# Kernel optimization log

Hardware: AMD Instinct MI355X
Metric: run time of the kernel (lower is better)

## Reference

```python
import jax, jax.numpy as jnp
import numpy as np

BS = 2
EMBED = 256
NH = 8
NL = 4
NP = 4
HD = EMBED // NH
SHAPES = [(128, 128), (64, 64), (32, 32), (16, 16)]
NQ = sum(h * w for h, w in SHAPES)  # 21760


def setup_inputs() -> dict:
    key = jax.random.key(0)
    ks = jax.random.split(key, 12)
    s = 1.0 / np.sqrt(EMBED)
    return {
        "query": jax.random.normal(ks[0], (BS, NQ, EMBED), jnp.float32),
        "reference_points": jax.random.uniform(ks[1], (BS, NQ, NL, 2), jnp.float32),
        "value": jax.random.normal(ks[2], (BS, NQ, EMBED), jnp.float32),
        "W_off": jax.random.normal(ks[3], (EMBED, NH * NL * NP * 2), jnp.float32) * 0.01,
        "b_off": jax.random.normal(ks[4], (NH * NL * NP * 2,), jnp.float32) * 0.5,
        "W_attn": jax.random.normal(ks[5], (EMBED, NH * NL * NP), jnp.float32) * 0.02,
        "b_attn": jnp.zeros((NH * NL * NP,), jnp.float32),
        "W_v": jax.random.normal(ks[6], (EMBED, EMBED), jnp.float32) * s,
        "b_v": jnp.zeros((EMBED,), jnp.float32),
        "W_out": jax.random.normal(ks[7], (EMBED, EMBED), jnp.float32) * s,
        "b_out": jnp.zeros((EMBED,), jnp.float32),
        "value_spatial_shapes": np.asarray(SHAPES, dtype=np.int64),
    }


def _ms_deform_attn(value, shapes, loc, aw):
    # value: [bs,V,nh,d]; loc: [bs,nq,nh,L,P,2] in [0,1]; aw: [bs,nq,nh,L,P]
    bs, V, nh, d = value.shape
    nq = loc.shape[1]
    out = jnp.zeros((bs, nq, nh, d), value.dtype)
    start = 0
    b_idx = jnp.arange(bs)[:, None, None, None]
    h_idx = jnp.arange(nh)[None, None, :, None]
    for l, (H, W) in enumerate(shapes):
        H, W = int(H), int(W)
        v = value[:, start:start + H * W].reshape(bs, H, W, nh, d)
        start += H * W
        g = 2.0 * loc[:, :, :, l] - 1.0  # [bs,nq,nh,P,2], grid_sample convention
        # align_corners=False pixel coordinates
        x = ((g[..., 0] + 1.0) * W - 1.0) * 0.5
        y = ((g[..., 1] + 1.0) * H - 1.0) * 0.5
        x0 = jnp.floor(x); y0 = jnp.floor(y)
        wx1 = x - x0; wx0 = 1.0 - wx1
        wy1 = y - y0; wy0 = 1.0 - wy1

        def gather(yi, xi):
            inb = (yi >= 0) & (yi < H) & (xi >= 0) & (xi < W)
            yc = jnp.clip(yi, 0, H - 1).astype(jnp.int32)
            xc = jnp.clip(xi, 0, W - 1).astype(jnp.int32)
            vals = v[b_idx, yc, xc, h_idx]  # [bs,nq,nh,P,d]
            return vals * inb[..., None].astype(v.dtype)

        samp = (gather(y0, x0) * (wy0 * wx0)[..., None]
                + gather(y0, x0 + 1) * (wy0 * wx1)[..., None]
                + gather(y0 + 1, x0) * (wy1 * wx0)[..., None]
                + gather(y0 + 1, x0 + 1) * (wy1 * wx1)[..., None])
        out = out + jnp.einsum('bqhpd,bqhp->bqhd', samp, aw[:, :, :, l])
    return out.reshape(bs, nq, nh * d)


def reference(query, reference_points, value, W_off, b_off, W_attn, b_attn,
              W_v, b_v, W_out, b_out, value_spatial_shapes):
    shapes = np.asarray(value_spatial_shapes)  # static [L,2]
    bs, nq, _ = query.shape
    v = (value @ W_v + b_v).reshape(bs, -1, NH, HD)
    off = (query @ W_off + b_off).reshape(bs, nq, NH, NL, NP, 2)
    aw = (query @ W_attn + b_attn).reshape(bs, nq, NH, NL * NP)
    aw = jax.nn.softmax(aw, axis=-1).reshape(bs, nq, NH, NL, NP)
    # offset normalizer: (W,H) per level
    norm = jnp.asarray(shapes[:, ::-1].astype(np.float32))  # [L,2]
    loc = reference_points[:, :, None, :, None, :] + off / norm[None, None, None, :, None, :]
    out = _ms_deform_attn(v, shapes, loc, aw)
    return out @ W_out + b_out
```

## Files before the change

### kernel.cpp

```cpp
#include <hip/hip_runtime.h>
#include <math.h>

#define BS 2
#define NQ 21760
#define V_LEN 21760
#define EMBED 256
#define NH 8
#define NL 4
#define NP 4
#define HD 32

typedef __bf16 bf16;
typedef __bf16 bf16x8 __attribute__((ext_vector_type(8)));
typedef __bf16 bf16x4 __attribute__((ext_vector_type(4)));
typedef float f32x4 __attribute__((ext_vector_type(4)));
typedef float f32x2 __attribute__((ext_vector_type(2)));
typedef unsigned int u32;

#define GLOAD_LDS16(gp, lp_) \
    __builtin_amdgcn_global_load_lds( \
        (const __attribute__((address_space(1))) unsigned int*)(gp), \
        (__attribute__((address_space(3))) unsigned int*)(lp_), 16, 0, 0)

__global__ __launch_bounds__(256) void cast_all(
    const float* __restrict__ W_v, const float* __restrict__ W_off,
    const float* __restrict__ W_attn, const float* __restrict__ W_out,
    const float* __restrict__ b_off, const float* __restrict__ b_attn,
    bf16* __restrict__ WTv, bf16* __restrict__ WToa, bf16* __restrict__ WTu,
    float* __restrict__ bcat)
{
    const int bid = blockIdx.x;
    const int tid = threadIdx.x;
    if (bid == 56) {
        if (tid < 384) bcat[tid] = (tid < 256) ? b_off[tid] : b_attn[tid - 256];
        return;
    }
    const float* W; bf16* WT; int N, tile;
    if (bid < 16)      { W = W_v;    WT = WTv;           N = 256; tile = bid; }
    else if (bid < 32) { W = W_off;  WT = WToa;          N = 256; tile = bid - 16; }
    else if (bid < 40) { W = W_attn; WT = WToa + 65536;  N = 128; tile = bid - 32; }
    else               { W = W_out;  WT = WTu;           N = 256; tile = bid - 40; }
    const int ntn = N >> 6;
    const int k0 = (tile / ntn) * 64, n0 = (tile % ntn) * 64;

    __shared__ float lds[64][65];
    const int c = tid & 63, r4 = tid >> 6;
    #pragma unroll
    for (int p = 0; p < 16; p++) {
        int rr = r4 + p * 4;
        lds[rr][c] = W[(size_t)(k0 + rr) * N + n0 + c];
    }
    __syncthreads();
    #pragma unroll
    for (int p = 0; p < 16; p++) {
        int i = r4 + p * 4;
        WT[(size_t)(n0 + i) * 256 + k0 + c] = (bf16)lds[c][i];
    }
}

template<bool A_F32, int OUT_MODE>
__global__ __launch_bounds__(256) void gemm_mfma(
    const void* __restrict__ Av, const bf16* __restrict__ WT,
    const float* __restrict__ bias, void* __restrict__ Cv,
    int N, int K, int ntn)
{
    const int nmt = gridDim.x / ntn;
    const int bmt = blockIdx.x % nmt;
    const int bnt = blockIdx.x / nmt;
    const int bm = bmt * 128, bn = bnt * 128;

    __shared__ __align__(16) bf16 Bs[2][128 * 32];
    __shared__ __align__(16) unsigned char AsRaw[2][A_F32 ? 128 * 32 * 4
                                                         : 128 * 32 * 2];

    const int tid = threadIdx.x;
    const int lane = tid & 63, wv = tid >> 6;
    const int wr = wv >> 1, wc = wv & 1;
    const int quad = lane >> 4, l16 = lane & 15;

    f32x4 acc[4][4];
    #pragma unroll
    for (int i = 0; i < 4; i++)
        #pragma unroll
        for (int j = 0; j < 4; j++)
            acc[i][j] = (f32x4){0.f, 0.f, 0.f, 0.f};

    const int b_row = tid >> 2, b_chunk = tid & 3;
    const int a_row8 = tid >> 3, a_phys = tid & 7;
    constexpr int NB = A_F32 ? 6 : 4;

    auto stage = [&](int buf, int k0) {
        if constexpr (A_F32) {
            const float* A = (const float*)Av;
            #pragma unroll
            for (int p = 0; p < 4; p++) {
                int row = a_row8 + p * 32;
                int csrc = a_phys ^ (row & 7);
                GLOAD_LDS16(&A[(size_t)(bm + row) * K + k0 + csrc * 4],
                            &AsRaw[buf][p * 4096 + tid * 16]);
            }
        } else {
            const bf16* A = (const bf16*)Av;
            #pragma unroll
            for (int p = 0; p < 2; p++) {
                int row = b_row + p * 64;
                GLOAD_LDS16(&A[(size_t)(bm + row) * K + k0 + b_chunk * 8],
                            &AsRaw[buf][p * 4096 + tid * 16]);
            }
        }
        #pragma unroll
        for (int p = 0; p < 2; p++) {
            int row = b_row + p * 64;
            GLOAD_LDS16(&WT[(size_t)(bn + row) * K + k0 + b_chunk * 8],
                        (unsigned char*)&Bs[buf][0] + p * 4096 + tid * 16);
        }
    };

    const int nt = K >> 5;
    stage(0, 0);
    int cur = 0;
    for (int t = 0; t < nt; t++) {
        __builtin_amdgcn_s_barrier();
        if (t + 1 < nt) {
            stage(cur ^ 1, (t + 1) << 5);
            asm volatile("s_waitcnt vmcnt(%0)" :: "n"(NB) : "memory");
        } else {
            asm volatile("s_waitcnt vmcnt(0)" ::: "memory");
        }
        __builtin_amdgcn_s_barrier();

        bf16x8 af[4], bfr[4];
        if constexpr (A_F32) {
            const float* Asf = (const float*)&AsRaw[cur][0];
            #pragma unroll
            for (int mi = 0; mi < 4; mi++) {
                int r = wr * 64 + mi * 16 + l16;
                int g = r & 7;
                f32x4 u0 = *(const f32x4*)&Asf[r * 32 + ((2 * quad) ^ g) * 4];
                f32x4 u1 = *(const f32x4*)&Asf[r * 32 + ((2 * quad + 1) ^ g) * 4];
                bf16x8 hh;
                hh[0] = (bf16)u0[0]; hh[1] = (bf16)u0[1]; hh[2] = (bf16)u0[2]; hh[3] = (bf16)u0[3];
                hh[4] = (bf16)u1[0]; hh[5] = (bf16)u1[1]; hh[6] = (bf16)u1[2]; hh[7] = (bf16)u1[3];
                af[mi] = hh;
            }
        } else {
            const bf16* Asb = (const bf16*)&AsRaw[cur][0];
            #pragma unroll
            for (int mi = 0; mi < 4; mi++) {
                int r = wr * 64 + mi * 16 + l16;
                af[mi] = *(const bf16x8*)&Asb[r * 32 + quad * 8];
            }
        }
        #pragma unroll
        for (int ni = 0; ni < 4; ni++) {
            int r = wc * 64 + ni * 16 + l16;
            bfr[ni] = *(const bf16x8*)&Bs[cur][r * 32 + quad * 8];
        }
        #pragma unroll
        for (int mi = 0; mi < 4; mi++)
            #pragma unroll
            for (int ni = 0; ni < 4; ni++)
                acc[mi][ni] = __builtin_amdgcn_mfma_f32_16x16x32_bf16(
                    af[mi], bfr[ni], acc[mi][ni], 0, 0, 0);
        cur ^= 1;
    }

    #pragma unroll
    for (int mi = 0; mi < 4; mi++) {
        #pragma unroll
        for (int ni = 0; ni < 4; ni++) {
            const int col = bn + wc * 64 + ni * 16 + l16;
            const int row0 = bm + wr * 64 + mi * 16 + quad * 4;
            const float bc = bias[col];
            #pragma unroll
            for (int r = 0; r < 4; r++) {
                float v = acc[mi][ni][r] + bc;
                if constexpr (OUT_MODE == 0) {
                    ((float*)Cv)[(size_t)(row0 + r) * N + col] = v;
                } else if constexpr (OUT_MODE == 1) {
                    ((bf16*)Cv)[(size_t)(row0 + r) * N + col] = (bf16)v;
                } else {
                    int rv = row0 + r;
                    int bb = (rv >= V_LEN) ? 1 : 0;
                    int vv = rv - bb * V_LEN;
                    ((bf16*)Cv)[((size_t)(bb * NH + (col >> 5)) * V_LEN + vv) * 32
                                + (col & 31)] = (bf16)v;
                }
            }
        }
    }
}

__device__ inline void acc8(const uint4& rr, float ww,
                            f32x2& a01, f32x2& a23, f32x2& a45, f32x2& a67)
{
    f32x2 v;
    v[0] = __uint_as_float(rr.x << 16); v[1] = __uint_as_float(rr.x & 0xFFFF0000u); a01 += v * ww;
    v[0] = __uint_as_float(rr.y << 16); v[1] = __uint_as_float(rr.y & 0xFFFF0000u); a23 += v * ww;
    v[0] = __uint_as_float(rr.z << 16); v[1] = __uint_as_float(rr.z & 0xFFFF0000u); a45 += v * ww;
    v[0] = __uint_as_float(rr.w << 16); v[1] = __uint_as_float(rr.w & 0xFFFF0000u); a67 += v * ww;
}

__global__ __launch_bounds__(256) void deform_head(
    const bf16* __restrict__ vproj, const float* __restrict__ offaw,
    const float* __restrict__ refp, bf16* __restrict__ sampled)
{
    const int gid = blockIdx.x;
    const int idx8 = gid & 7;
    const int mid = gid >> 3;
    const int qg = mid % (NQ / 16);
    const int hsel = mid / (NQ / 16);
    const int h = (idx8 >> 1) + (hsel << 2);
    const int b = idx8 & 1;

    const int wv = threadIdx.x >> 6;
    const int t = threadIdx.x & 63;
    const int qq = t >> 4, s = t & 15;
    const int q = qg * 16 + wv * 4 + qq;
    const int bq = b * NQ + q;
    const int wq = wv * 4 + qq;

    __shared__ __align__(16) float s_w[16][16][4];
    __shared__ int s_idx[16][16];

    const float* row = offaw + (size_t)bq * 384;

    float lg = row[256 + h * 16 + s];
    float m = lg;
    m = fmaxf(m, __shfl_xor(m, 1));
    m = fmaxf(m, __shfl_xor(m, 2));
    m = fmaxf(m, __shfl_xor(m, 4));
    m = fmaxf(m, __shfl_xor(m, 8));
    float ev = __expf(lg - m);
    float ssum = ev;
    ssum += __shfl_xor(ssum, 1);
    ssum += __shfl_xor(ssum, 2);
    ssum += __shfl_xor(ssum, 4);
    ssum += __shfl_xor(ssum, 8);
    float aw = ev * (1.0f / ssum);

    {
        int l = s >> 2;
        int Wl = 128 >> l, Hl = Wl;
        int st = (l == 0) ? 0 : (l == 1) ? 16384 : (l == 2) ? 20480 : 21504;
        float2 rp = *(const float2*)&refp[((size_t)bq * 4 + l) * 2];
        float2 oxy = *(const float2*)&row[h * 32 + s * 2];
        float fW = (float)Wl, fH = (float)Hl;
        float x = (rp.x + oxy.x / fW) * fW - 0.5f;
        float y = (rp.y + oxy.y / fH) * fH - 0.5f;
        float xf = floorf(x), yf = floorf(y);
        int x0 = (int)xf, y0 = (int)yf;
        float wx1 = x - xf, wx0 = 1.f - wx1;
        float wy1 = y - yf, wy0 = 1.f - wy1;
        float wx0p = ((x0 >= 0) && (x0 < Wl)) ? wx0 : 0.f;
        float wx1p = ((x0 + 1 >= 0) && (x0 + 1 < Wl)) ? wx1 : 0.f;
        float wy0p = ((y0 >= 0) && (y0 < Hl)) ? wy0 : 0.f;
        float wy1p = ((y0 + 1 >= 0) && (y0 + 1 < Hl)) ? wy1 : 0.f;
        int px = min(max(x0, 0), Wl - 2), py = min(max(y0, 0), Hl - 2);
        int cx0 = min(max(x0, 0), Wl - 1), cx1 = min(max(x0 + 1, 0), Wl - 1);
        int cy0 = min(max(y0, 0), Hl - 1), cy1 = min(max(y0 + 1, 0), Hl - 1);
        float sx0 = ((cx0 == px) ? wx0p : 0.f) + ((cx1 == px) ? wx1p : 0.f);
        float sx1 = ((cx0 == px + 1) ? wx0p : 0.f) + ((cx1 == px + 1) ? wx1p : 0.f);
        float sy0 = ((cy0 == py) ? wy0p : 0.f) + ((cy1 == py) ? wy1p : 0.f);
        float sy1 = ((cy0 == py + 1) ? wy0p : 0.f) + ((cy1 == py + 1) ? wy1p : 0.f);
        s_idx[wq][s] = st + py * Wl + px;
        s_w[wq][s][0] = sy0 * sx0 * aw;
        s_w[wq][s][1] = sy0 * sx1 * aw;
        s_w[wq][s][2] = sy1 * sx0 * aw;
        s_w[wq][s][3] = sy1 * sx1 * aw;
    }

    const int chgrp = t & 3;
    const int xslot = (t >> 2) & 1;
    const int rowsel = (t >> 3) & 1;
    const int widx = rowsel * 2 + xslot;
    const bf16* vb = vproj + (size_t)(b * NH + h) * V_LEN * 32;

    f32x2 a01 = {0.f, 0.f}, a23 = {0.f, 0.f}, a45 = {0.f, 0.f}, a67 = {0.f, 0.f};
    #pragma unroll
    for (int i = 0; i < 16; i++) {
        const int Wl = 128 >> (i >> 2);
        int base = s_idx[wq][i];
        float w = s_w[wq][i][widx];
        const bf16* p = vb + (size_t)(base + rowsel * Wl + xslot) * 32 + chgrp * 8;
        uint4 r = *(const uint4*)p;
        acc8(r, w, a01, a23, a45, a67);
    }

    float sarr[8] = {a01[0], a01[1], a23[0], a23[1], a45[0], a45[1], a67[0], a67[1]};
    #pragma unroll
    for (int i = 0; i < 8; i++) {
        sarr[i] += __shfl_xor(sarr[i], 4);
        sarr[i] += __shfl_xor(sarr[i], 8);
    }

    if ((t & 12) == 0) {
        bf16x8 o;
        #pragma unroll
        for (int i = 0; i < 8; i++) o[i] = (bf16)sarr[i];
        *(bf16x8*)&sampled[(size_t)bq * 256 + h * 32 + chgrp * 8] = o;
    }
}

extern "C" void kernel_launch(void* const* d_in, const int* in_sizes, int n_in,
                              void* d_out, int out_size, void* d_ws, size_t ws_size,
                              hipStream_t stream)
{
    const float* query  = (const float*)d_in[0];
    const float* refp   = (const float*)d_in[1];
    const float* value  = (const float*)d_in[2];
    const float* W_off  = (const float*)d_in[3];
    const float* b_off  = (const float*)d_in[4];
    const float* W_attn = (const float*)d_in[5];
    const float* b_attn = (const float*)d_in[6];
    const float* W_v    = (const float*)d_in[7];
    const float* b_v    = (const float*)d_in[8];
    const float* W_out  = (const float*)d_in[9];
    const float* b_out  = (const float*)d_in[10];
    float* out = (float*)d_out;

    const int M = BS * NQ;

    char* ws = (char*)d_ws;
    bf16*  WTv   = (bf16*)ws;                      ws += 256 * 256 * 2;
    bf16*  WToa  = (bf16*)ws;                      ws += 384 * 256 * 2;
    bf16*  WTu   = (bf16*)ws;                      ws += 256 * 256 * 2;
    float* bcat  = (float*)ws;                     ws += 384 * 4;
    bf16*  vproj = (bf16*)ws;                      ws += (size_t)M * 256 * 2;
    float* offaw = (float*)ws;                     ws += (size_t)M * 384 * 4;
    bf16*  samp  = (bf16*)ws;                      ws += (size_t)M * 256 * 2;

    cast_all<<<57, 256, 0, stream>>>(W_v, W_off, W_attn, W_out, b_off, b_attn,
                                     WTv, WToa, WTu, bcat);

    gemm_mfma<true, 2><<<(M / 128) * 2, 256, 0, stream>>>(value, WTv, b_v, vproj, 256, 256, 2);
    gemm_mfma<true, 0><<<(M / 128) * 3, 256, 0, stream>>>(query, WToa, bcat, offaw, 384, 256, 3);
    deform_head<<<2 * NH * (NQ / 16), 256, 0, stream>>>(vproj, offaw, refp, samp);
    gemm_mfma<false, 0><<<(M / 128) * 2, 256, 0, stream>>>(samp, WTu, b_out, out, 256, 256, 2);
}
```

Before: 268.6 us.

## Load GEMM weights directly to registers and double per-thread work in deform sampling

After: 275.5 us. +2.6%, slower.

```diff
diff --git a/kernel.cpp b/kernel.cpp
--- a/kernel.cpp
+++ b/kernel.cpp
@@ -62,14 +62,13 @@
 __global__ __launch_bounds__(256) void gemm_mfma(
     const void* __restrict__ Av, const bf16* __restrict__ WT,
     const float* __restrict__ bias, void* __restrict__ Cv,
-    int N, int K, int ntn)
+    int N, int ntn)
 {
     const int nmt = gridDim.x / ntn;
     const int bmt = blockIdx.x % nmt;
     const int bnt = blockIdx.x / nmt;
     const int bm = bmt * 128, bn = bnt * 128;
 
-    __shared__ __align__(16) bf16 Bs[2][128 * 32];
     __shared__ __align__(16) unsigned char AsRaw[2][A_F32 ? 128 * 32 * 4
                                                          : 128 * 32 * 2];
 
@@ -87,7 +86,12 @@
 
     const int b_row = tid >> 2, b_chunk = tid & 3;
     const int a_row8 = tid >> 3, a_phys = tid & 7;
-    constexpr int NB = A_F32 ? 6 : 4;
+    constexpr int NA = A_F32 ? 4 : 2;
+
+    const bf16* bB[4];
+    #pragma unroll
+    for (int ni = 0; ni < 4; ni++)
+        bB[ni] = WT + (size_t)(bn + wc * 64 + ni * 16 + l16) * 256 + quad * 8;
 
     auto stage = [&](int buf, int k0) {
         if constexpr (A_F32) {
@@ -96,7 +100,7 @@
             for (int p = 0; p < 4; p++) {
                 int row = a_row8 + p * 32;
                 int csrc = a_phys ^ (row & 7);
-                GLOAD_LDS16(&A[(size_t)(bm + row) * K + k0 + csrc * 4],
+                GLOAD_LDS16(&A[(size_t)(bm + row) * 256 + k0 + csrc * 4],
                             &AsRaw[buf][p * 4096 + tid * 16]);
             }
         } else {
@@ -104,32 +108,30 @@
             #pragma unroll
             for (int p = 0; p < 2; p++) {
                 int row = b_row + p * 64;
-                GLOAD_LDS16(&A[(size_t)(bm + row) * K + k0 + b_chunk * 8],
+                GLOAD_LDS16(&A[(size_t)(bm + row) * 256 + k0 + b_chunk * 8],
                             &AsRaw[buf][p * 4096 + tid * 16]);
             }
-        }
-        #pragma unroll
-        for (int p = 0; p < 2; p++) {
-            int row = b_row + p * 64;
-            GLOAD_LDS16(&WT[(size_t)(bn + row) * K + k0 + b_chunk * 8],
-                        (unsigned char*)&Bs[buf][0] + p * 4096 + tid * 16);
         }
     };
 
-    const int nt = K >> 5;
     stage(0, 0);
     int cur = 0;
-    for (int t = 0; t < nt; t++) {
+    #pragma unroll
+    for (int t = 0; t < 8; t++) {
         __builtin_amdgcn_s_barrier();
-        if (t + 1 < nt) {
-            stage(cur ^ 1, (t + 1) << 5);
-            asm volatile("s_waitcnt vmcnt(%0)" :: "n"(NB) : "memory");
+        bf16x8 bfr[4];
+        #pragma unroll
+        for (int ni = 0; ni < 4; ni++)
+            bfr[ni] = *(const bf16x8*)(bB[ni] + t * 32);
+        if (t < 7) {
+            stage(cur ^ 1, (t + 1) * 32);
+            asm volatile("s_waitcnt vmcnt(%0)" :: "n"(NA + 4) : "memory");
         } else {
-            asm volatile("s_waitcnt vmcnt(0)" ::: "memory");
+            asm volatile("s_waitcnt vmcnt(4)" ::: "memory");
         }
         __builtin_amdgcn_s_barrier();
 
-        bf16x8 af[4], bfr[4];
+        bf16x8 af[4];
         if constexpr (A_F32) {
             const float* Asf = (const float*)&AsRaw[cur][0];
             #pragma unroll
@@ -150,11 +152,6 @@
                 int r = wr * 64 + mi * 16 + l16;
                 af[mi] = *(const bf16x8*)&Asb[r * 32 + quad * 8];
             }
-        }
-        #pragma unroll
-        for (int ni = 0; ni < 4; ni++) {
-            int r = wc * 64 + ni * 16 + l16;
-            bfr[ni] = *(const bf16x8*)&Bs[cur][r * 32 + quad * 8];
         }
         #pragma unroll
         for (int mi = 0; mi < 4; mi++)
@@ -208,43 +205,45 @@
     const int gid = blockIdx.x;
     const int idx8 = gid & 7;
     const int mid = gid >> 3;
-    const int qg = mid % (NQ / 16);
-    const int hsel = mid / (NQ / 16);
+    const int qg = mid % (NQ / 32);
+    const int hsel = mid / (NQ / 32);
     const int h = (idx8 >> 1) + (hsel << 2);
     const int b = idx8 & 1;
 
     const int wv = threadIdx.x >> 6;
     const int t = threadIdx.x & 63;
-    const int qq = t >> 4, s = t & 15;
-    const int q = qg * 16 + wv * 4 + qq;
+    const int qq = t >> 3, e = t & 7;
+    const int wq = wv * 8 + qq;
+    const int q = qg * 32 + wq;
     const int bq = b * NQ + q;
-    const int wq = wv * 4 + qq;
-
-    __shared__ __align__(16) float s_w[16][16][4];
-    __shared__ int s_idx[16][16];
+
+    __shared__ int   s_idx[32][17];
+    __shared__ __align__(16) float s_w[32][17][4];
 
     const float* row = offaw + (size_t)bq * 384;
 
-    float lg = row[256 + h * 16 + s];
-    float m = lg;
+    float l0 = row[256 + h * 16 + e];
+    float l1 = row[256 + h * 16 + e + 8];
+    float m = fmaxf(l0, l1);
     m = fmaxf(m, __shfl_xor(m, 1));
     m = fmaxf(m, __shfl_xor(m, 2));
     m = fmaxf(m, __shfl_xor(m, 4));
-    m = fmaxf(m, __shfl_xor(m, 8));
-    float ev = __expf(lg - m);
-    float ssum = ev;
+    float e0 = __expf(l0 - m), e1 = __expf(l1 - m);
+    float ssum = e0 + e1;
     ssum += __shfl_xor(ssum, 1);
     ssum += __shfl_xor(ssum, 2);
     ssum += __shfl_xor(ssum, 4);
-    ssum += __shfl_xor(ssum, 8);
-    float aw = ev * (1.0f / ssum);
-
-    {
-        int l = s >> 2;
+    float rs = 1.0f / ssum;
+    float awv[2] = {e0 * rs, e1 * rs};
+
+    #pragma unroll
+    for (int sI = 0; sI < 2; sI++) {
+        int lp = e + sI * 8;
+        int l = lp >> 2;
         int Wl = 128 >> l, Hl = Wl;
         int st = (l == 0) ? 0 : (l == 1) ? 16384 : (l == 2) ? 20480 : 21504;
         float2 rp = *(const float2*)&refp[((size_t)bq * 4 + l) * 2];
-        float2 oxy = *(const float2*)&row[h * 32 + s * 2];
+        float2 oxy = *(const float2*)&row[h * 32 + lp * 2];
         float fW = (float)Wl, fH = (float)Hl;
         float x = (rp.x + oxy.x / fW) * fW - 0.5f;
         float y = (rp.y + oxy.y / fH) * fH - 0.5f;
@@ -252,6 +251,7 @@
         int x0 = (int)xf, y0 = (int)yf;
         float wx1 = x - xf, wx0 = 1.f - wx1;
         float wy1 = y - yf, wy0 = 1.f - wy1;
+        float aw = awv[sI];
         float wx0p = ((x0 >= 0) && (x0 < Wl)) ? wx0 : 0.f;
         float wx1p = ((x0 + 1 >= 0) && (x0 + 1 < Wl)) ? wx1 : 0.f;
         float wy0p = ((y0 >= 0) && (y0 < Hl)) ? wy0 : 0.f;
@@ -263,38 +263,35 @@
         float sx1 = ((cx0 == px + 1) ? wx0p : 0.f) + ((cx1 == px + 1) ? wx1p : 0.f);
         float sy0 = ((cy0 == py) ? wy0p : 0.f) + ((cy1 == py) ? wy1p : 0.f);
         float sy1 = ((cy0 == py + 1) ? wy0p : 0.f) + ((cy1 == py + 1) ? wy1p : 0.f);
-        s_idx[wq][s] = st + py * Wl + px;
-        s_w[wq][s][0] = sy0 * sx0 * aw;
-        s_w[wq][s][1] = sy0 * sx1 * aw;
-        s_w[wq][s][2] = sy1 * sx0 * aw;
-        s_w[wq][s][3] = sy1 * sx1 * aw;
-    }
-
-    const int chgrp = t & 3;
-    const int xslot = (t >> 2) & 1;
-    const int rowsel = (t >> 3) & 1;
-    const int widx = rowsel * 2 + xslot;
-    const bf16* vb = vproj + (size_t)(b * NH + h) * V_LEN * 32;
+        s_idx[wq][lp] = (st + py * Wl + px) * 64;
+        s_w[wq][lp][0] = sy0 * sx0 * aw;
+        s_w[wq][lp][1] = sy1 * sx0 * aw;
+        s_w[wq][lp][2] = sy0 * sx1 * aw;
+        s_w[wq][lp][3] = sy1 * sx1 * aw;
+    }
+
+    const int j = t & 7;
+    const int xslot = j >> 2, chgrp = j & 3;
+    const char* vb = (const char*)vproj + (size_t)(b * NH + h) * V_LEN * 64;
+    const int voffbase = j * 16;
 
     f32x2 a01 = {0.f, 0.f}, a23 = {0.f, 0.f}, a45 = {0.f, 0.f}, a67 = {0.f, 0.f};
     #pragma unroll
     for (int i = 0; i < 16; i++) {
         const int Wl = 128 >> (i >> 2);
-        int base = s_idx[wq][i];
-        float w = s_w[wq][i][widx];
-        const bf16* p = vb + (size_t)(base + rowsel * Wl + xslot) * 32 + chgrp * 8;
-        uint4 r = *(const uint4*)p;
-        acc8(r, w, a01, a23, a45, a67);
+        int off = s_idx[wq][i] + voffbase;
+        f32x2 wp = *(const f32x2*)&s_w[wq][i][xslot * 2];
+        uint4 r0 = *(const uint4*)(vb + off);
+        uint4 r1 = *(const uint4*)(vb + off + Wl * 64);
+        acc8(r0, wp[0], a01, a23, a45, a67);
+        acc8(r1, wp[1], a01, a23, a45, a67);
     }
 
     float sarr[8] = {a01[0], a01[1], a23[0], a23[1], a45[0], a45[1], a67[0], a67[1]};
     #pragma unroll
-    for (int i = 0; i < 8; i++) {
-        sarr[i] += __shfl_xor(sarr[i], 4);
-        sarr[i] += __shfl_xor(sarr[i], 8);
-    }
-
-    if ((t & 12) == 0) {
+    for (int i = 0; i < 8; i++) sarr[i] += __shfl_xor(sarr[i], 4);
+
+    if ((t & 4) == 0) {
         bf16x8 o;
         #pragma unroll
         for (int i = 0; i < 8; i++) o[i] = (bf16)sarr[i];
@@ -333,8 +330,8 @@
     cast_all<<<57, 256, 0, stream>>>(W_v, W_off, W_attn, W_out, b_off, b_attn,
                                      WTv, WToa, WTu, bcat);
 
-    gemm_mfma<true, 2><<<(M / 128) * 2, 256, 0, stream>>>(value, WTv, b_v, vproj, 256, 256, 2);
-    gemm_mfma<true, 0><<<(M / 128) * 3, 256, 0, stream>>>(query, WToa, bcat, offaw, 384, 256, 3);
-    deform_head<<<2 * NH * (NQ / 16), 256, 0, stream>>>(vproj, offaw, refp, samp);
-    gemm_mfma<false, 0><<<(M / 128) * 2, 256, 0, stream>>>(samp, WTu, b_out, out, 256, 256, 2);
-}
+    gemm_mfma<true, 2><<<(M / 128) * 2, 256, 0, stream>>>(value, WTv, b_v, vproj, 256, 2);
+    gemm_mfma<true, 0><<<(M / 128) * 3, 256, 0, stream>>>(query, WToa, bcat, offaw, 384, 3);
+    deform_head<<<2 * NH * (NQ / 32), 256, 0, stream>>>(vproj, offaw, refp, samp);
+    gemm_mfma<false, 0><<<(M / 128) * 2, 256, 0, stream>>>(samp, WTu, b_out, out, 256, 2);
+}
```
